# Kernel optimization log

Measured on AMD Instinct MI355X. Metric: run time of the kernel, lower is better.

Reference implementation:

```python
import jax, jax.numpy as jnp
import numpy as np

N_NODES = 100000
N_EDGES = 1600000


def setup_inputs() -> dict:
    key = jax.random.key(0)
    ks = jax.random.split(key, 12)
    s = lambda d: 1.0 / np.sqrt(d)
    inp = {
        "x": jax.random.normal(ks[0], (N_NODES, 64), dtype=jnp.float32),
        "edge_index": jax.random.randint(ks[1], (2, N_EDGES), 0, N_NODES, dtype=jnp.int64),
        "W_embed": jax.random.normal(ks[2], (64, 128), dtype=jnp.float32) * s(64),
        "eps1": jnp.zeros((), jnp.float32),
        "w1a": jax.random.normal(ks[3], (128, 128), dtype=jnp.float32) * s(128),
        "b1a": jnp.zeros((128,), jnp.float32),
        "w1b": jax.random.normal(ks[4], (128, 128), dtype=jnp.float32) * s(128),
        "b1b": jnp.zeros((128,), jnp.float32),
        "eps2": jnp.zeros((), jnp.float32),
        "w2a": jax.random.normal(ks[5], (128, 256), dtype=jnp.float32) * s(128),
        "b2a": jnp.zeros((256,), jnp.float32),
        "w2b": jax.random.normal(ks[6], (256, 128), dtype=jnp.float32) * s(256),
        "b2b": jnp.zeros((128,), jnp.float32),
        "eps3": jnp.zeros((), jnp.float32),
        "w3a": jax.random.normal(ks[7], (128, 256), dtype=jnp.float32) * s(128),
        "b3a": jnp.zeros((256,), jnp.float32),
        "w3b": jax.random.normal(ks[8], (256, 128), dtype=jnp.float32) * s(256),
        "b3b": jnp.zeros((128,), jnp.float32),
    }
    return inp


def _aggregate(h, src, dst, n):
    # GINConv sum aggregation: out[i] = sum_{(j,i) in E} h[j]
    return jax.ops.segment_sum(h[src], dst, num_segments=n)


def reference(x, edge_index, W_embed, eps1, w1a, b1a, w1b, b1b,
              eps2, w2a, b2a, w2b, b2b, eps3, w3a, b3a, w3b, b3b):
    src, dst = edge_index[0], edge_index[1]
    n = x.shape[0]
    # node_attr_encoder: linear embedding (dropout p=0 -> identity)
    h = x @ W_embed  # [N, dim]
    # conv1: nn((1+eps)*h + sum_neighbors), nn = Lin->ReLU->Lin
    z = (1.0 + eps1) * h + _aggregate(h, src, dst, n)
    h = jax.nn.relu(z @ w1a + b1a) @ w1b + b1b
    # conv2/conv3: nn = Lin->ReLU->Lin->ReLU
    z = (1.0 + eps2) * h + _aggregate(h, src, dst, n)
    h = jax.nn.relu(jax.nn.relu(z @ w2a + b2a) @ w2b + b2b)
    z = (1.0 + eps3) * h + _aggregate(h, src, dst, n)
    h = jax.nn.relu(jax.nn.relu(z @ w3a + b3a) @ w3b + b3b)
    return h
```

## Files before the change

### kernel.cpp

```cpp
#include <hip/hip_runtime.h>
#include <hip/hip_bf16.h>
#include <stdint.h>


typedef __attribute__((ext_vector_type(8))) short short8;
typedef __attribute__((ext_vector_type(16))) float float16v;
typedef __attribute__((ext_vector_type(4))) unsigned int uint4v;

#define BKT 512
#define NBMAX 256

#define MFMA32 __builtin_amdgcn_mfma_f32_32x32x16_bf16

union U4S8 { uint4v u; short8 s; };

__device__ __forceinline__ float b2f_lo(unsigned int u) {
    return __uint_as_float(u << 16);
}
__device__ __forceinline__ float b2f_hi(unsigned int u) {
    return __uint_as_float(u & 0xffff0000u);
}
__device__ __forceinline__ unsigned short f2b(float f) {
    unsigned int u = __float_as_uint(f);
    return (unsigned short)((u + 0x7fffu + ((u >> 16) & 1u)) >> 16);
}
__device__ __forceinline__ unsigned cvtpk_bf16(float a, float b) {
    unsigned r;
    asm("v_cvt_pk_bf16_f32 %0, %1, %2" : "=v"(r) : "v"(a), "v"(b));
    return r;
}
__device__ __forceinline__ void perm32swap(unsigned& a, unsigned& b) {
    asm("v_permlane32_swap_b32 %0, %1" : "+v"(a), "+v"(b));
}

__global__ void detect_i64_kernel(const unsigned int* ei, int* flag) {
    if (threadIdx.x == 0) {
        int is64 = 1;
        for (int e = 0; e < 64; ++e)
            if (ei[2 * e + 1] != 0u) { is64 = 0; break; }
        *flag = is64;
    }
}

__device__ __forceinline__ int edge_at(const int* ei32, int is64, long long pos) {
    if (is64) return (int)(((const long long*)ei32)[pos]);
    return ei32[pos];
}

__global__ __launch_bounds__(256) void part_hist_kernel(
        const int* __restrict__ ei, const int* __restrict__ flag,
        int* __restrict__ bh, int E, int NB, int PB) {
    __shared__ int h[NBMAX];
    const int g = blockIdx.x, tid = threadIdx.x;
    const int is64 = *flag;
    for (int i = tid; i < NB; i += 256) h[i] = 0;
    __syncthreads();
    const int e0 = g * PB, e1 = min(e0 + PB, E);
    for (int e = e0 + tid; e < e1; e += 256) {
        int d = edge_at(ei, is64, (long long)E + e);
        atomicAdd(&h[d >> 9], 1);
    }
    __syncthreads();
    for (int i = tid; i < NB; i += 256) bh[i * gridDim.x + g] = h[i];
}

__global__ __launch_bounds__(1024) void scan1_kernel(
        const int* __restrict__ in, int* __restrict__ out,
        int* __restrict__ partial, int n) {
    __shared__ int sm[1024];
    const int t = threadIdx.x;
    const int i = blockIdx.x * 1024 + t;
    int v = (i < n) ? in[i] : 0;
    sm[t] = v;
    __syncthreads();
#pragma unroll
    for (int off = 1; off < 1024; off <<= 1) {
        int x = (t >= off) ? sm[t - off] : 0;
        __syncthreads();
        sm[t] += x;
        __syncthreads();
    }
    if (i < n) out[i] = sm[t] - v;
    if (t == 1023) partial[blockIdx.x] = sm[1023];
}

__global__ __launch_bounds__(256) void scan2_kernel(
        int* __restrict__ partial, int* __restrict__ blockoff, int g1) {
    __shared__ int sm[256];
    const int t = threadIdx.x;
    int v = (t < g1) ? partial[t] : 0;
    sm[t] = v;
    __syncthreads();
#pragma unroll
    for (int off = 1; off < 256; off <<= 1) {
        int x = (t >= off) ? sm[t - off] : 0;
        __syncthreads();
        sm[t] += x;
        __syncthreads();
    }
    blockoff[t] = sm[t] - v;
}

__global__ __launch_bounds__(1024) void scan3g_kernel(
        int* __restrict__ a, const int* __restrict__ blockoff, int n) {
    int i = blockIdx.x * 1024 + threadIdx.x;
    if (i < n) a[i] += blockoff[blockIdx.x];
}

__global__ __launch_bounds__(256) void part_scatter_kernel(
        const int* __restrict__ ei, const int* __restrict__ flag,
        const int* __restrict__ bhs, unsigned int* __restrict__ staged,
        int E, int NB, int PB) {
    __shared__ int cur[NBMAX];
    const int g = blockIdx.x, tid = threadIdx.x;
    const int is64 = *flag;
    for (int i = tid; i < NB; i += 256) cur[i] = bhs[i * gridDim.x + g];
    __syncthreads();
    const int e0 = g * PB, e1 = min(e0 + PB, E);
    for (int e = e0 + tid; e < e1; e += 256) {
        int d = edge_at(ei, is64, (long long)E + e);
        int s = edge_at(ei, is64, (long long)e);
        int b = d >> 9;
        int p = atomicAdd(&cur[b], 1);
        staged[p] = ((unsigned int)(d & (BKT - 1)) << 17) | (unsigned int)s;
    }
}

__global__ __launch_bounds__(256) void csr_local_kernel(
        const unsigned int* __restrict__ staged, const int* __restrict__ bhs,
        int* __restrict__ offs, int* __restrict__ csr, int N, int E, int NB, int G2) {
    __shared__ int hist[BKT];
    __shared__ int cur[BKT];
    const int b = blockIdx.x;
    const int tid = threadIdx.x;
    const int start = bhs[b * G2];
    const int end = (b + 1 < NB) ? bhs[(b + 1) * G2] : E;
    const int node0 = b * BKT;
    for (int i = tid; i < BKT; i += 256) hist[i] = 0;
    __syncthreads();
    for (int i = start + tid; i < end; i += 256)
        atomicAdd(&hist[staged[i] >> 17], 1);
    __syncthreads();
    const int i0 = tid * 2, i1 = i0 + 1;
    for (int off = 1; off < BKT; off <<= 1) {
        int v0 = (i0 >= off) ? hist[i0 - off] : 0;
        int v1 = (i1 >= off) ? hist[i1 - off] : 0;
        __syncthreads();
        hist[i0] += v0;
        hist[i1] += v1;
        __syncthreads();
    }
    for (int i = tid; i < BKT; i += 256) {
        int node = node0 + i;
        if (node < N) {
            int e0 = start + ((i == 0) ? 0 : hist[i - 1]);
            offs[node] = e0;
            cur[i] = e0;
        }
    }
    if (b == NB - 1 && tid == 0) offs[N] = E;
    __syncthreads();
    for (int i = start + tid; i < end; i += 256) {
        unsigned int v = staged[i];
        int dl = v >> 17;
        int src = (int)(v & 0x1ffff);
        int p = atomicAdd(&cur[dl], 1);
        csr[p] = src;
    }
}

struct PW { const float* W; unsigned short* o; int K; int KOUT; };
struct PWAll { PW d[7]; int cum[8]; };

__global__ __launch_bounds__(256) void packall_kernel(PWAll P) {
    int id = blockIdx.x * blockDim.x + threadIdx.x;
    if (id >= P.cum[7]) return;
    int w = 0;
#pragma unroll
    for (int k = 1; k < 7; ++k) w += (id >= P.cum[k]);
    const int local = id - P.cum[w];
    const float* W = P.d[w].W;
    unsigned short* out = P.d[w].o;
    const int K = P.d[w].K, KOUT = P.d[w].KOUT;
    const int KS = K / 16;
    const int l = local & 63;
    const int s = (local >> 6) % KS;
    const int T = local / (KS * 64);
    const int kbase = s * 16 + ((l >> 5) << 3);
    const int n = T * 32 + (l & 31);
#pragma unroll
    for (int j = 0; j < 8; ++j)
        out[(long long)local * 8 + j] = f2b(W[(long long)(kbase + j) * KOUT + n]);
}

__global__ __launch_bounds__(256) void mm_embed(
        const float* __restrict__ X, const unsigned short* __restrict__ Wp,
        unsigned short* __restrict__ out, int Mreal) {
    constexpr int KS = 4;
    const int tid = threadIdx.x;
    const int w = tid >> 6;
    const int l = tid & 63;
    const int lm = l & 31;
    const int lk = l >> 5;
    const int wr = w & 1, wc = w >> 1;
    const long long R0 = (long long)blockIdx.x * 128 + wr * 64;
    const int T0 = (wc * 64) >> 5;

    const long long r0 = (R0 + lm < Mreal) ? (R0 + lm) : (Mreal - 1);
    const long long r1 = (R0 + 32 + lm < Mreal) ? (R0 + 32 + lm) : (Mreal - 1);
    const float* xr0 = X + r0 * 64 + lk * 8;
    const float* xr1 = X + r1 * 64 + lk * 8;
    const unsigned short* bb0 = Wp + ((long long)T0 * KS * 64 + l) * 8;
    const unsigned short* bb1 = Wp + ((long long)(T0 + 1) * KS * 64 + l) * 8;

    float16v acc00 = {}, acc01 = {}, acc10 = {}, acc11 = {};
#pragma unroll
    for (int s = 0; s < KS; ++s) {
        float4 f0a = *(const float4*)(xr0 + s * 16);
        float4 f0b = *(const float4*)(xr0 + s * 16 + 4);
        float4 f1a = *(const float4*)(xr1 + s * 16);
        float4 f1b = *(const float4*)(xr1 + s * 16 + 4);
        short8 a0, a1;
        a0[0] = (short)f2b(f0a.x); a0[1] = (short)f2b(f0a.y);
        a0[2] = (short)f2b(f0a.z); a0[3] = (short)f2b(f0a.w);
        a0[4] = (short)f2b(f0b.x); a0[5] = (short)f2b(f0b.y);
        a0[6] = (short)f2b(f0b.z); a0[7] = (short)f2b(f0b.w);
        a1[0] = (short)f2b(f1a.x); a1[1] = (short)f2b(f1a.y);
        a1[2] = (short)f2b(f1a.z); a1[3] = (short)f2b(f1a.w);
        a1[4] = (short)f2b(f1b.x); a1[5] = (short)f2b(f1b.y);
        a1[6] = (short)f2b(f1b.z); a1[7] = (short)f2b(f1b.w);
        short8 b0 = *(const short8*)(bb0 + (long long)s * 64 * 8);
        short8 b1 = *(const short8*)(bb1 + (long long)s * 64 * 8);
        acc00 = MFMA32(a0, b0, acc00, 0, 0, 0);
        acc01 = MFMA32(a0, b1, acc01, 0, 0, 0);
        acc10 = MFMA32(a1, b0, acc10, 0, 0, 0);
        acc11 = MFMA32(a1, b1, acc11, 0, 0, 0);
    }
    auto st = [&](float16v acc, long long rb, int col) {
#pragma unroll
        for (int r = 0; r < 16; ++r) {
            long long row = rb + (r & 3) + 8 * (r >> 2);
            out[row * 128 + col] = f2b(acc[r]);
        }
    };
    const long long rbase = R0 + 4 * lk;
    st(acc00, rbase,      wc * 64 + lm);
    st(acc01, rbase,      wc * 64 + 32 + lm);
    st(acc10, rbase + 32, wc * 64 + lm);
    st(acc11, rbase + 32, wc * 64 + 32 + lm);
}

__global__ __launch_bounds__(256) void aggz_kernel(
        const unsigned short* __restrict__ H, const int* __restrict__ offs,
        const int* __restrict__ csr, const float* __restrict__ eps,
        unsigned short* __restrict__ Z, int n) {
    const int node = blockIdx.x * 16 + (threadIdx.x >> 4);
    const int c8 = (threadIdx.x & 15) << 3;
    if (node >= n) return;
    const int beg = offs[node];
    const int end = offs[node + 1];
    float a0 = 0.f, a1 = 0.f, a2 = 0.f, a3 = 0.f;
    float a4 = 0.f, a5 = 0.f, a6 = 0.f, a7 = 0.f;
    int i = beg;
    for (; i + 3 < end; i += 4) {
        const int j0 = csr[i], j1 = csr[i + 1], j2 = csr[i + 2], j3 = csr[i + 3];
        const uint4 u0 = *(const uint4*)(H + ((long long)j0 << 7) + c8);
        const uint4 u1 = *(const uint4*)(H + ((long long)j1 << 7) + c8);
        const uint4 u2 = *(const uint4*)(H + ((long long)j2 << 7) + c8);
        const uint4 u3 = *(const uint4*)(H + ((long long)j3 << 7) + c8);
        a0 += (b2f_lo(u0.x) + b2f_lo(u1.x)) + (b2f_lo(u2.x) + b2f_lo(u3.x));
        a1 += (b2f_hi(u0.x) + b2f_hi(u1.x)) + (b2f_hi(u2.x) + b2f_hi(u3.x));
        a2 += (b2f_lo(u0.y) + b2f_lo(u1.y)) + (b2f_lo(u2.y) + b2f_lo(u3.y));
        a3 += (b2f_hi(u0.y) + b2f_hi(u1.y)) + (b2f_hi(u2.y) + b2f_hi(u3.y));
        a4 += (b2f_lo(u0.z) + b2f_lo(u1.z)) + (b2f_lo(u2.z) + b2f_lo(u3.z));
        a5 += (b2f_hi(u0.z) + b2f_hi(u1.z)) + (b2f_hi(u2.z) + b2f_hi(u3.z));
        a6 += (b2f_lo(u0.w) + b2f_lo(u1.w)) + (b2f_lo(u2.w) + b2f_lo(u3.w));
        a7 += (b2f_hi(u0.w) + b2f_hi(u1.w)) + (b2f_hi(u2.w) + b2f_hi(u3.w));
    }
    for (; i < end; ++i) {
        const uint4 u0 = *(const uint4*)(H + ((long long)csr[i] << 7) + c8);
        a0 += b2f_lo(u0.x); a1 += b2f_hi(u0.x);
        a2 += b2f_lo(u0.y); a3 += b2f_hi(u0.y);
        a4 += b2f_lo(u0.z); a5 += b2f_hi(u0.z);
        a6 += b2f_lo(u0.w); a7 += b2f_hi(u0.w);
    }
    const uint4 uh = *(const uint4*)(H + ((long long)node << 7) + c8);
    const float e = 1.0f + eps[0];
    a0 = fmaf(e, b2f_lo(uh.x), a0); a1 = fmaf(e, b2f_hi(uh.x), a1);
    a2 = fmaf(e, b2f_lo(uh.y), a2); a3 = fmaf(e, b2f_hi(uh.y), a3);
    a4 = fmaf(e, b2f_lo(uh.z), a4); a5 = fmaf(e, b2f_hi(uh.z), a5);
    a6 = fmaf(e, b2f_lo(uh.w), a6); a7 = fmaf(e, b2f_hi(uh.w), a7);
    uint4 o;
    o.x = ((unsigned int)f2b(a1) << 16) | (unsigned int)f2b(a0);
    o.y = ((unsigned int)f2b(a3) << 16) | (unsigned int)f2b(a2);
    o.z = ((unsigned int)f2b(a5) << 16) | (unsigned int)f2b(a4);
    o.w = ((unsigned int)f2b(a7) << 16) | (unsigned int)f2b(a6);
    *(uint4*)(Z + ((long long)node << 7) + c8) = o;
}


#define CVT_TO_PA(ACC, CBASE) do {                                     \
        unsigned X1 = cvtpk_bf16((ACC)[0], (ACC)[1]);                  \
        unsigned Y1 = cvtpk_bf16((ACC)[4], (ACC)[5]);                  \
        unsigned X2 = cvtpk_bf16((ACC)[2], (ACC)[3]);                  \
        unsigned Y2 = cvtpk_bf16((ACC)[6], (ACC)[7]);                  \
        perm32swap(X1, Y1); perm32swap(X2, Y2);                        \
        U4S8 u0; u0.u[0] = X1; u0.u[1] = X2; u0.u[2] = Y1; u0.u[3] = Y2; \
        pa[(CBASE)] = u0.s;                                            \
        unsigned X3 = cvtpk_bf16((ACC)[8], (ACC)[9]);                  \
        unsigned Y3 = cvtpk_bf16((ACC)[12], (ACC)[13]);                \
        unsigned X4 = cvtpk_bf16((ACC)[10], (ACC)[11]);                \
        unsigned Y4 = cvtpk_bf16((ACC)[14], (ACC)[15]);                \
        perm32swap(X3, Y3); perm32swap(X4, Y4);                        \
        U4S8 u1; u1.u[0] = X3; u1.u[1] = X4; u1.u[2] = Y3; u1.u[3] = Y4; \
        pa[(CBASE) + 1] = u1.s;                                        \
    } while (0)

template<int KMID, bool RELU2, bool OUTF32>
__global__ __launch_bounds__(256, 2) void fused_mlp2(
        const unsigned short* __restrict__ Zin,
        const unsigned short* __restrict__ Wap, const float* __restrict__ ba,
        const unsigned short* __restrict__ Wbp, const float* __restrict__ bb,
        void* __restrict__ outp, int Mreal, int nstrips) {
    constexpr int NF = KMID / 32;
    constexpr int NCH = KMID / 16;
    const int tid = threadIdx.x;
    const int wid = tid >> 6;
    const int l = tid & 63;
    const int lo = l & 31;
    const int hi = l >> 5;
    const int strip = blockIdx.x * 4 + wid;
    if (strip >= nstrips) return;
    const long long node0 = (long long)strip * 32;

    long long zr = node0 + lo;
    if (zr >= Mreal) zr = Mreal - 1;
    const unsigned short* zrow = Zin + zr * 128 + hi * 8;
    short8 z[8];
#pragma unroll
    for (int s = 0; s < 8; ++s) z[s] = *(const short8*)(zrow + s * 16);

    short8 pa[NCH];

#pragma unroll
    for (int fp = 0; fp < NF / 2; ++fp) {
        const int f0 = 2 * fp, f1 = 2 * fp + 1;
        float16v accA, accB;
#pragma unroll
        for (int q = 0; q < 4; ++q) {
            const float4 tA = *(const float4*)(ba + f0 * 32 + q * 8 + hi * 4);
            const float4 tB = *(const float4*)(ba + f1 * 32 + q * 8 + hi * 4);
            accA[4 * q + 0] = tA.x; accA[4 * q + 1] = tA.y;
            accA[4 * q + 2] = tA.z; accA[4 * q + 3] = tA.w;
            accB[4 * q + 0] = tB.x; accB[4 * q + 1] = tB.y;
            accB[4 * q + 2] = tB.z; accB[4 * q + 3] = tB.w;
        }
        const unsigned short* wa0 = Wap + ((long long)f0 * 8 * 64 + l) * 8;
        const unsigned short* wa1 = Wap + ((long long)f1 * 8 * 64 + l) * 8;
#pragma unroll
        for (int s = 0; s < 8; ++s) {
            short8 a0 = *(const short8*)(wa0 + (long long)s * 64 * 8);
            short8 a1 = *(const short8*)(wa1 + (long long)s * 64 * 8);
            accA = MFMA32(a0, z[s], accA, 0, 0, 0);
            accB = MFMA32(a1, z[s], accB, 0, 0, 0);
        }
#pragma unroll
        for (int r = 0; r < 16; ++r) {
            accA[r] = fmaxf(accA[r], 0.f);
            accB[r] = fmaxf(accB[r], 0.f);
        }
        CVT_TO_PA(accA, 4 * fp);
        CVT_TO_PA(accB, 4 * fp + 2);
    }

    float16v acc2[4] = {};
#pragma unroll
    for (int c = 0; c < NCH; ++c) {
#pragma unroll
        for (int g = 0; g < 4; ++g) {
            short8 b = *(const short8*)(Wbp + ((long long)(g * NCH + c) * 64 + l) * 8);
            acc2[g] = MFMA32(pa[c], b, acc2[g], 0, 0, 0);
        }
    }

#pragma unroll
    for (int g = 0; g < 4; ++g) {
        const int col = g * 32 + lo;
        const float bv = bb[col];
#pragma unroll
        for (int r = 0; r < 16; ++r) {
            float v = acc2[g][r] + bv;
            if (RELU2) v = fmaxf(v, 0.f);
            const long long node = node0 + (r & 3) + 8 * (r >> 2) + 4 * hi;
            if (node < Mreal) {
                if (OUTF32) ((float*)outp)[node * 128 + col] = v;
                else ((unsigned short*)outp)[node * 128 + col] = f2b(v);
            }
        }
    }
}

extern "C" void kernel_launch(void* const* d_in, const int* in_sizes, int n_in,
                              void* d_out, int out_size, void* d_ws, size_t ws_size,
                              hipStream_t stream) {
    const float* x    = (const float*)d_in[0];
    const int*   ei   = (const int*)d_in[1];
    const float* Wemb = (const float*)d_in[2];
    const float* eps1 = (const float*)d_in[3];
    const float* w1a  = (const float*)d_in[4];
    const float* b1a  = (const float*)d_in[5];
    const float* w1b  = (const float*)d_in[6];
    const float* b1b  = (const float*)d_in[7];
    const float* eps2 = (const float*)d_in[8];
    const float* w2a  = (const float*)d_in[9];
    const float* b2a  = (const float*)d_in[10];
    const float* w2b  = (const float*)d_in[11];
    const float* b2b  = (const float*)d_in[12];
    const float* eps3 = (const float*)d_in[13];
    const float* w3a  = (const float*)d_in[14];
    const float* b3a  = (const float*)d_in[15];
    const float* w3b  = (const float*)d_in[16];
    const float* b3b  = (const float*)d_in[17];

    const int N = in_sizes[0] / 64;
    const int E = in_sizes[1] / 2;
    const int Mpad = ((N + 127) / 128) * 128;
    const int NB = (N + BKT - 1) / BKT;
    const int G2 = 1024;
    const int PB = (E + G2 - 1) / G2;
    const int BH = NB * G2;

    char* ws = (char*)d_ws;
    size_t off = 0;
    auto alloc = [&](size_t bytes) -> void* {
        void* p = ws + off;
        off = (off + bytes + 255) & ~(size_t)255;
        return p;
    };
    unsigned short* Ha  = (unsigned short*)alloc((size_t)Mpad * 128 * 2);
    unsigned short* Hb2 = (unsigned short*)alloc((size_t)Mpad * 128 * 2);
    unsigned short* Zb  = (unsigned short*)alloc((size_t)Mpad * 128 * 2);
    unsigned short* pWe = (unsigned short*)alloc((size_t)64 * 128 * 2);
    unsigned short* p1a = (unsigned short*)alloc((size_t)128 * 128 * 2);
    unsigned short* p1b = (unsigned short*)alloc((size_t)128 * 128 * 2);
    unsigned short* p2a = (unsigned short*)alloc((size_t)128 * 256 * 2);
    unsigned short* p2b = (unsigned short*)alloc((size_t)256 * 128 * 2);
    unsigned short* p3a = (unsigned short*)alloc((size_t)128 * 256 * 2);
    unsigned short* p3b = (unsigned short*)alloc((size_t)256 * 128 * 2);
    int* offs = (int*)alloc((size_t)(N + 1) * 4);
    int* csr  = (int*)alloc((size_t)E * 4);
    unsigned int* staged = (unsigned int*)alloc((size_t)E * 4);
    int* bh   = (int*)alloc((size_t)BH * 4);
    int* bhs  = (int*)alloc((size_t)BH * 4);
    int* part = (int*)alloc(1024);
    int* boff = (int*)alloc(1024);
    int* flag = (int*)alloc(256);

    detect_i64_kernel<<<1, 64, 0, stream>>>((const unsigned int*)ei, flag);
    part_hist_kernel<<<G2, 256, 0, stream>>>(ei, flag, bh, E, NB, PB);
    const int G1 = (BH + 1023) / 1024;
    scan1_kernel<<<G1, 1024, 0, stream>>>(bh, bhs, part, BH);
    scan2_kernel<<<1, 256, 0, stream>>>(part, boff, G1);
    scan3g_kernel<<<G1, 1024, 0, stream>>>(bhs, boff, BH);
    part_scatter_kernel<<<G2, 256, 0, stream>>>(ei, flag, bhs, staged, E, NB, PB);
    csr_local_kernel<<<NB, 256, 0, stream>>>(staged, bhs, offs, csr, N, E, NB, G2);

    {
        PWAll P;
        const PW descs[7] = {
            {Wemb, pWe, 64, 128}, {w1a, p1a, 128, 128}, {w1b, p1b, 128, 128},
            {w2a, p2a, 128, 256}, {w2b, p2b, 256, 128}, {w3a, p3a, 128, 256},
            {w3b, p3b, 256, 128}};
        int c = 0;
        for (int k = 0; k < 7; ++k) {
            P.d[k] = descs[k];
            P.cum[k] = c;
            c += (descs[k].KOUT / 32) * (descs[k].K / 16) * 64;
        }
        P.cum[7] = c;
        packall_kernel<<<(c + 255) / 256, 256, 0, stream>>>(P);
    }

    const int MMB = Mpad / 128;
    const int AGB = (N + 15) / 16;
    const int NSTRIP = (N + 31) / 32;
    const int MLPB = (NSTRIP + 3) / 4;

    mm_embed<<<MMB, 256, 0, stream>>>(x, pWe, Ha, N);

    aggz_kernel<<<AGB, 256, 0, stream>>>(Ha, offs, csr, eps1, Zb, N);
    fused_mlp2<128, false, false><<<MLPB, 256, 0, stream>>>(Zb, p1a, b1a, p1b, b1b, Hb2, N, NSTRIP);

    aggz_kernel<<<AGB, 256, 0, stream>>>(Hb2, offs, csr, eps2, Zb, N);
    fused_mlp2<256, true, false><<<MLPB, 256, 0, stream>>>(Zb, p2a, b2a, p2b, b2b, Ha, N, NSTRIP);

    aggz_kernel<<<AGB, 256, 0, stream>>>(Ha, offs, csr, eps3, Zb, N);
    fused_mlp2<256, true, true><<<MLPB, 256, 0, stream>>>(Zb, p3a, b3a, p3b, b3b, d_out, N, NSTRIP);
}
```

Before: 517.1 us.

## Stage MLP weights in LDS with persistent grid and prefetched Z strips

Rewrites the fused two-layer MLP kernel as a persistent kernel: 256 blocks of 512 threads copy both packed weight matrices and biases into shared memory once, then loop over 32-node strips. The next strip's Z rows are prefetched during the last first-layer chunk, and the second GEMM is interleaved per chunk so the full hidden activation no longer has to stay in registers. The aim is to remove repeated global and L2 weight reads per strip and to lower register pressure. In exchange it uses up to 128 KB of LDS per block for KMID=256, which caps occupancy and adds a startup copy per block.

```diff
diff --git a/kernel.cpp b/kernel.cpp
--- a/kernel.cpp
+++ b/kernel.cpp
@@ -299,103 +299,140 @@
 }
 
 
-#define CVT_TO_PA(ACC, CBASE) do {                                     \
+#define CVT_TO_PA2(ACC, P0, P1) do {                                   \
         unsigned X1 = cvtpk_bf16((ACC)[0], (ACC)[1]);                  \
         unsigned Y1 = cvtpk_bf16((ACC)[4], (ACC)[5]);                  \
         unsigned X2 = cvtpk_bf16((ACC)[2], (ACC)[3]);                  \
         unsigned Y2 = cvtpk_bf16((ACC)[6], (ACC)[7]);                  \
         perm32swap(X1, Y1); perm32swap(X2, Y2);                        \
         U4S8 u0; u0.u[0] = X1; u0.u[1] = X2; u0.u[2] = Y1; u0.u[3] = Y2; \
-        pa[(CBASE)] = u0.s;                                            \
+        (P0) = u0.s;                                                   \
         unsigned X3 = cvtpk_bf16((ACC)[8], (ACC)[9]);                  \
         unsigned Y3 = cvtpk_bf16((ACC)[12], (ACC)[13]);                \
         unsigned X4 = cvtpk_bf16((ACC)[10], (ACC)[11]);                \
         unsigned Y4 = cvtpk_bf16((ACC)[14], (ACC)[15]);                \
         perm32swap(X3, Y3); perm32swap(X4, Y4);                        \
         U4S8 u1; u1.u[0] = X3; u1.u[1] = X4; u1.u[2] = Y3; u1.u[3] = Y4; \
-        pa[(CBASE) + 1] = u1.s;                                        \
+        (P1) = u1.s;                                                   \
     } while (0)
 
 template<int KMID, bool RELU2, bool OUTF32>
-__global__ __launch_bounds__(256, 2) void fused_mlp2(
+__global__ __launch_bounds__(512, 2) void fused_mlp3(
         const unsigned short* __restrict__ Zin,
         const unsigned short* __restrict__ Wap, const float* __restrict__ ba,
         const unsigned short* __restrict__ Wbp, const float* __restrict__ bb,
         void* __restrict__ outp, int Mreal, int nstrips) {
     constexpr int NF = KMID / 32;
     constexpr int NCH = KMID / 16;
+    constexpr int WAS = 128 * KMID;
+    __shared__ unsigned short wlds[KMID * 256];
+    __shared__ float blds[KMID + 128];
     const int tid = threadIdx.x;
+
+    {
+        const uint4* sa = (const uint4*)Wap;
+        const uint4* sb = (const uint4*)Wbp;
+        uint4* da = (uint4*)wlds;
+        uint4* db = (uint4*)(wlds + WAS);
+#pragma unroll
+        for (int i = tid; i < KMID * 16; i += 512) { da[i] = sa[i]; db[i] = sb[i]; }
+        for (int i = tid; i < KMID; i += 512) blds[i] = ba[i];
+        if (tid < 128) blds[KMID + tid] = bb[tid];
+    }
+    __syncthreads();
+
     const int wid = tid >> 6;
     const int l = tid & 63;
     const int lo = l & 31;
     const int hi = l >> 5;
-    const int strip = blockIdx.x * 4 + wid;
+    const int stride = gridDim.x * 8;
+    int strip = blockIdx.x * 8 + wid;
     if (strip >= nstrips) return;
-    const long long node0 = (long long)strip * 32;
-
-    long long zr = node0 + lo;
-    if (zr >= Mreal) zr = Mreal - 1;
-    const unsigned short* zrow = Zin + zr * 128 + hi * 8;
-    short8 z[8];
-#pragma unroll
-    for (int s = 0; s < 8; ++s) z[s] = *(const short8*)(zrow + s * 16);
-
-    short8 pa[NCH];
-
-#pragma unroll
-    for (int fp = 0; fp < NF / 2; ++fp) {
-        const int f0 = 2 * fp, f1 = 2 * fp + 1;
-        float16v accA, accB;
-#pragma unroll
-        for (int q = 0; q < 4; ++q) {
-            const float4 tA = *(const float4*)(ba + f0 * 32 + q * 8 + hi * 4);
-            const float4 tB = *(const float4*)(ba + f1 * 32 + q * 8 + hi * 4);
-            accA[4 * q + 0] = tA.x; accA[4 * q + 1] = tA.y;
-            accA[4 * q + 2] = tA.z; accA[4 * q + 3] = tA.w;
-            accB[4 * q + 0] = tB.x; accB[4 * q + 1] = tB.y;
-            accB[4 * q + 2] = tB.z; accB[4 * q + 3] = tB.w;
+
+    auto zload = [&](int s_, short8* zz) {
+        long long zr = (long long)s_ * 32 + lo;
+        if (zr >= Mreal) zr = Mreal - 1;
+        const unsigned short* zrow = Zin + zr * 128 + hi * 8;
+#pragma unroll
+        for (int s = 0; s < 8; ++s) zz[s] = *(const short8*)(zrow + s * 16);
+    };
+
+    short8 zc[8];
+    zload(strip, zc);
+
+    while (strip < nstrips) {
+        const int nxt = strip + stride;
+        float16v acc2[4] = {};
+        short8 zn[8];
+
+#pragma unroll
+        for (int fp = 0; fp < NF / 2; ++fp) {
+            if (fp == NF / 2 - 1) {
+                if (nxt < nstrips) zload(nxt, zn);
+            }
+            const int f0 = 2 * fp, f1 = f0 + 1;
+            float16v accA, accB;
+#pragma unroll
+            for (int q = 0; q < 4; ++q) {
+                const float4 tA = *(const float4*)(blds + f0 * 32 + q * 8 + hi * 4);
+                const float4 tB = *(const float4*)(blds + f1 * 32 + q * 8 + hi * 4);
+                accA[4 * q + 0] = tA.x; accA[4 * q + 1] = tA.y;
+                accA[4 * q + 2] = tA.z; accA[4 * q + 3] = tA.w;
+                accB[4 * q + 0] = tB.x; accB[4 * q + 1] = tB.y;
+                accB[4 * q + 2] = tB.z; accB[4 * q + 3] = tB.w;
+            }
+            const unsigned short* wa0 = wlds + ((long long)(f0 * 8) * 64 + l) * 8;
+            const unsigned short* wa1 = wlds + ((long long)(f1 * 8) * 64 + l) * 8;
+#pragma unroll
+            for (int s = 0; s < 8; ++s) {
+                short8 a0 = *(const short8*)(wa0 + s * 64 * 8);
+                short8 a1 = *(const short8*)(wa1 + s * 64 * 8);
+                accA = MFMA32(a0, zc[s], accA, 0, 0, 0);
+                accB = MFMA32(a1, zc[s], accB, 0, 0, 0);
+            }
+#pragma unroll
+            for (int r = 0; r < 16; ++r) {
+                accA[r] = fmaxf(accA[r], 0.f);
+                accB[r] = fmaxf(accB[r], 0.f);
+            }
+            short8 pa0, pa1, pa2, pa3;
+            CVT_TO_PA2(accA, pa0, pa1);
+            CVT_TO_PA2(accB, pa2, pa3);
+            const unsigned short* wb = wlds + WAS + ((long long)(fp * 4) * 64 + l) * 8;
+#pragma unroll
+            for (int g = 0; g < 4; ++g) {
+                const unsigned short* wbg = wb + (long long)g * NCH * 64 * 8;
+                short8 b0 = *(const short8*)(wbg);
+                short8 b1 = *(const short8*)(wbg + 64 * 8);
+                short8 b2 = *(const short8*)(wbg + 2 * 64 * 8);
+                short8 b3 = *(const short8*)(wbg + 3 * 64 * 8);
+                acc2[g] = MFMA32(pa0, b0, acc2[g], 0, 0, 0);
+                acc2[g] = MFMA32(pa1, b1, acc2[g], 0, 0, 0);
+                acc2[g] = MFMA32(pa2, b2, acc2[g], 0, 0, 0);
+                acc2[g] = MFMA32(pa3, b3, acc2[g], 0, 0, 0);
+            }
         }
-        const unsigned short* wa0 = Wap + ((long long)f0 * 8 * 64 + l) * 8;
-        const unsigned short* wa1 = Wap + ((long long)f1 * 8 * 64 + l) * 8;
-#pragma unroll
-        for (int s = 0; s < 8; ++s) {
-            short8 a0 = *(const short8*)(wa0 + (long long)s * 64 * 8);
-            short8 a1 = *(const short8*)(wa1 + (long long)s * 64 * 8);
-            accA = MFMA32(a0, z[s], accA, 0, 0, 0);
-            accB = MFMA32(a1, z[s], accB, 0, 0, 0);
+
+#pragma unroll
+        for (int g = 0; g < 4; ++g) {
+            const int col = g * 32 + lo;
+            const float bv = blds[KMID + col];
+#pragma unroll
+            for (int r = 0; r < 16; ++r) {
+                float v = acc2[g][r] + bv;
+                if (RELU2) v = fmaxf(v, 0.f);
+                const long long node = (long long)strip * 32 + (r & 3) + 8 * (r >> 2) + 4 * hi;
+                if (node < Mreal) {
+                    if (OUTF32) ((float*)outp)[node * 128 + col] = v;
+                    else ((unsigned short*)outp)[node * 128 + col] = f2b(v);
+                }
+            }
         }
-#pragma unroll
-        for (int r = 0; r < 16; ++r) {
-            accA[r] = fmaxf(accA[r], 0.f);
-            accB[r] = fmaxf(accB[r], 0.f);
-        }
-        CVT_TO_PA(accA, 4 * fp);
-        CVT_TO_PA(accB, 4 * fp + 2);
-    }
-
-    float16v acc2[4] = {};
-#pragma unroll
-    for (int c = 0; c < NCH; ++c) {
-#pragma unroll
-        for (int g = 0; g < 4; ++g) {
-            short8 b = *(const short8*)(Wbp + ((long long)(g * NCH + c) * 64 + l) * 8);
-            acc2[g] = MFMA32(pa[c], b, acc2[g], 0, 0, 0);
-        }
-    }
-
-#pragma unroll
-    for (int g = 0; g < 4; ++g) {
-        const int col = g * 32 + lo;
-        const float bv = bb[col];
-#pragma unroll
-        for (int r = 0; r < 16; ++r) {
-            float v = acc2[g][r] + bv;
-            if (RELU2) v = fmaxf(v, 0.f);
-            const long long node = node0 + (r & 3) + 8 * (r >> 2) + 4 * hi;
-            if (node < Mreal) {
-                if (OUTF32) ((float*)outp)[node * 128 + col] = v;
-                else ((unsigned short*)outp)[node * 128 + col] = f2b(v);
-            }
+
+        strip = nxt;
+        if (strip < nstrips) {
+#pragma unroll
+            for (int s = 0; s < 8; ++s) zc[s] = zn[s];
         }
     }
 }
@@ -484,16 +521,16 @@
     const int MMB = Mpad / 128;
     const int AGB = (N + 15) / 16;
     const int NSTRIP = (N + 31) / 32;
-    const int MLPB = (NSTRIP + 3) / 4;
+    const int MLPG = 256;
 
     mm_embed<<<MMB, 256, 0, stream>>>(x, pWe, Ha, N);
 
     aggz_kernel<<<AGB, 256, 0, stream>>>(Ha, offs, csr, eps1, Zb, N);
-    fused_mlp2<128, false, false><<<MLPB, 256, 0, stream>>>(Zb, p1a, b1a, p1b, b1b, Hb2, N, NSTRIP);
+    fused_mlp3<128, false, false><<<MLPG, 512, 0, stream>>>(Zb, p1a, b1a, p1b, b1b, Hb2, N, NSTRIP);
 
     aggz_kernel<<<AGB, 256, 0, stream>>>(Hb2, offs, csr, eps2, Zb, N);
-    fused_mlp2<256, true, false><<<MLPB, 256, 0, stream>>>(Zb, p2a, b2a, p2b, b2b, Ha, N, NSTRIP);
+    fused_mlp3<256, true, false><<<MLPG, 512, 0, stream>>>(Zb, p2a, b2a, p2b, b2b, Ha, N, NSTRIP);
 
     aggz_kernel<<<AGB, 256, 0, stream>>>(Ha, offs, csr, eps3, Zb, N);
-    fused_mlp2<256, true, true><<<MLPB, 256, 0, stream>>>(Zb, p3a, b3a, p3b, b3b, d_out, N, NSTRIP);
-}
+    fused_mlp3<256, true, true><<<MLPG, 512, 0, stream>>>(Zb, p3a, b3a, p3b, b3b, d_out, N, NSTRIP);
+}
```

Result: faster. 435.4 us (-15.8%).
